# Kernel optimization log

Measured on AMD Instinct MI355X. Metric: run time of the kernel, lower is better.

Reference implementation:

```python
import jax, jax.numpy as jnp
import numpy as np

FRAME_NUMBER = 16
FRAME_SIZE = 128
SAMPLE_NUM = 16
NUM_EVENTS = 1048576


def setup_inputs() -> dict:
    key = jax.random.key(0)
    k1, k2, k3, k4 = jax.random.split(key, 4)
    event_values = jax.random.normal(k1, (SAMPLE_NUM, NUM_EVENTS), dtype=jnp.float32)
    # indices rows: (t, x, y). t sorted ascending so torch's `indices[0, -1] + 1`
    # sizing logic is valid; x, y in [0, FRAME_SIZE).
    t_idx = jnp.sort(jax.random.randint(k2, (NUM_EVENTS,), 0, NUM_EVENTS // FRAME_NUMBER, dtype=jnp.int64))
    x_idx = jax.random.randint(k3, (NUM_EVENTS,), 0, FRAME_SIZE, dtype=jnp.int64)
    y_idx = jax.random.randint(k4, (NUM_EVENTS,), 0, FRAME_SIZE, dtype=jnp.int64)
    idx0 = jnp.stack([t_idx, x_idx, y_idx], axis=0)  # [3, num_events]
    # Module only reads event_indices[0]; replicate across samples for shape fidelity.
    event_indices = jnp.broadcast_to(idx0[None], (SAMPLE_NUM, 3, NUM_EVENTS))
    return {"event_values": event_values, "event_indices": event_indices, "use_soft": 0}


def reference(event_values, event_indices, use_soft):
    # Hard split by number (use_soft=False path).
    # coalesce over (t,x,y) + sparse.sum over t == scatter-add over (x,y) per window.
    S, N = event_values.shape
    F, FS = FRAME_NUMBER, FRAME_SIZE
    W = N // F  # time_window (events per frame)

    x_idx = event_indices[0, 1]  # [N], shared across samples (module uses indices[0])
    y_idx = event_indices[0, 2]  # [N]
    frame_id = jnp.arange(N, dtype=x_idx.dtype) // W  # which frame each event falls in
    seg = (frame_id * FS + x_idx) * FS + y_idx  # flat (frame, x, y) bin id, [N]

    pos = jax.nn.relu(event_values)   # [S, N]
    neg = jax.nn.relu(-event_values)  # [S, N]

    num_segments = F * FS * FS
    # segment_sum over events -> [F*FS*FS, S], then reshape to [F, X, Y, S]
    pos_f = jax.ops.segment_sum(pos.T, seg, num_segments=num_segments).reshape(F, FS, FS, S)
    neg_f = jax.ops.segment_sum(neg.T, seg, num_segments=num_segments).reshape(F, FS, FS, S)

    frames = jnp.stack([neg_f, pos_f], axis=1)  # [F, 2, X, Y, S]
    # torch: permute(-1,0,1,3,2) -> [S,F,2,Y,X], then transpose(0,1) -> [F,S,2,Y,X]
    return jnp.transpose(frames, (0, 4, 1, 3, 2))
```

## Files before the change

kernel.cpp:

```cpp
#include <hip/hip_runtime.h>

#define SAMPLES 16
#define NEVENTS (1 << 20)
#define FRAMES  16
#define FSZ     128
#define WIN     (NEVENTS / FRAMES)
#define BINS    (FSZ * FSZ)
#define TPB     1024
#define EPT     16
#define STEPS   (WIN / (EPT * TPB))

typedef float v4f __attribute__((ext_vector_type(4)));
typedef int   v4i __attribute__((ext_vector_type(4)));


__device__ __forceinline__ void prep4(v4f v, v4i xv, v4i yv, int* off, float* av) {
    const unsigned ux = __float_as_uint(v.x), uy = __float_as_uint(v.y),
                   uz = __float_as_uint(v.z), uw = __float_as_uint(v.w);
    off[0] = (int)((((~ux) >> 31) << 14) | ((unsigned)yv.x << 7) | (unsigned)xv.x);
    off[1] = (int)((((~uy) >> 31) << 14) | ((unsigned)yv.y << 7) | (unsigned)xv.y);
    off[2] = (int)((((~uz) >> 31) << 14) | ((unsigned)yv.z << 7) | (unsigned)xv.z);
    off[3] = (int)((((~uw) >> 31) << 14) | ((unsigned)yv.w << 7) | (unsigned)xv.w);
    av[0] = __builtin_fabsf(v.x);
    av[1] = __builtin_fabsf(v.y);
    av[2] = __builtin_fabsf(v.z);
    av[3] = __builtin_fabsf(v.w);
}

#define LOADSTEP(B, step)                                                        \
    v##B##0 = __builtin_nontemporal_load(&ev4[(step) * 4 * TPB + 0 * TPB + tid]);\
    v##B##1 = __builtin_nontemporal_load(&ev4[(step) * 4 * TPB + 1 * TPB + tid]);\
    v##B##2 = __builtin_nontemporal_load(&ev4[(step) * 4 * TPB + 2 * TPB + tid]);\
    v##B##3 = __builtin_nontemporal_load(&ev4[(step) * 4 * TPB + 3 * TPB + tid]);\
    x##B##0 = x4[(step) * 4 * TPB + 0 * TPB + tid];                              \
    x##B##1 = x4[(step) * 4 * TPB + 1 * TPB + tid];                              \
    x##B##2 = x4[(step) * 4 * TPB + 2 * TPB + tid];                              \
    x##B##3 = x4[(step) * 4 * TPB + 3 * TPB + tid];                              \
    y##B##0 = y4[(step) * 4 * TPB + 0 * TPB + tid];                              \
    y##B##1 = y4[(step) * 4 * TPB + 1 * TPB + tid];                              \
    y##B##2 = y4[(step) * 4 * TPB + 2 * TPB + tid];                              \
    y##B##3 = y4[(step) * 4 * TPB + 3 * TPB + tid];

#define PREP(B)                                                                  \
    prep4(v##B##0, x##B##0, y##B##0, &off[0],  &av[0]);                          \
    prep4(v##B##1, x##B##1, y##B##1, &off[4],  &av[4]);                          \
    prep4(v##B##2, x##B##2, y##B##2, &off[8],  &av[8]);                          \
    prep4(v##B##3, x##B##3, y##B##3, &off[12], &av[12]);

#define BURST()                                                                  \
    _Pragma("unroll")                                                            \
    for (int k = 0; k < 16; ++k) atomicAdd(&lds[off[k]], av[k]);

__global__ __launch_bounds__(TPB) void frame_accum_kernel(
    const float* __restrict__ ev,
    const int*   __restrict__ idx,
    float*       __restrict__ out)
{
    extern __shared__ float lds[];
    const int tid = threadIdx.x;
    const int s = blockIdx.x & (SAMPLES - 1);
    const int f = blockIdx.x >> 4;

    v4f* lds4 = (v4f*)lds;
    const v4f zero4 = (v4f)(0.f);
#pragma unroll
    for (int i = 0; i < (2 * BINS / 4) / TPB; ++i)
        lds4[i * TPB + tid] = zero4;
    __syncthreads();

    const v4f* ev4 = (const v4f*)(ev  + (size_t)s * NEVENTS + (size_t)f * WIN);
    const v4i* x4  = (const v4i*)(idx + (size_t)NEVENTS      + (size_t)f * WIN);
    const v4i* y4  = (const v4i*)(idx + (size_t)2 * NEVENTS  + (size_t)f * WIN);

    v4f vA0, vA1, vA2, vA3, vB0, vB1, vB2, vB3;
    v4i xA0, xA1, xA2, xA3, xB0, xB1, xB2, xB3;
    v4i yA0, yA1, yA2, yA3, yB0, yB1, yB2, yB3;
    int   off[16];
    float av[16];

    LOADSTEP(A, 0)
#pragma unroll
    for (int st = 0; st < STEPS; st += 2) {
        LOADSTEP(B, st + 1)
        PREP(A)
        BURST()
        if (st + 2 < STEPS) { LOADSTEP(A, st + 2) }
        PREP(B)
        BURST()
    }
    __syncthreads();

    v4f* op4 = (v4f*)(out + ((size_t)(f * SAMPLES + s)) * 2 * BINS);
#pragma unroll
    for (int i = 0; i < (2 * BINS / 4) / TPB; ++i)
        __builtin_nontemporal_store(lds4[i * TPB + tid], &op4[i * TPB + tid]);
}

extern "C" void kernel_launch(void* const* d_in, const int* in_sizes, int n_in,
                              void* d_out, int out_size, void* d_ws, size_t ws_size,
                              hipStream_t stream) {
    const float* ev  = (const float*)d_in[0];
    const int*   idx = (const int*)d_in[1];
    float* out = (float*)d_out;

    (void)hipFuncSetAttribute((const void*)frame_accum_kernel,
                              hipFuncAttributeMaxDynamicSharedMemorySize,
                              2 * BINS * (int)sizeof(float));

    frame_accum_kernel<<<FRAMES * SAMPLES, TPB, 2 * BINS * sizeof(float), stream>>>(
        ev, idx, out);
}
```

Before: 343.9 us.

## Split atomic accumulation between LDS and global workspace atomics

Adds a hybrid kernel that sends odd chunks of events to global-memory atomics in a zeroed workspace and even chunks to LDS atomics, then sums both at the end. The goal is to spread atomic contention across two hardware paths instead of serializing everything on LDS atomics. The main loop is also simplified to single-vector chunks with unroll 4, replacing the manual double-buffered prefetch. The cost is an extra memset of the output-sized workspace, global atomic traffic through L2, and an extra workspace read. The hybrid path runs only when a large enough workspace is provided; otherwise an LDS-only fallback runs.

```diff
diff --git a/kernel.cpp b/kernel.cpp
--- a/kernel.cpp
+++ b/kernel.cpp
@@ -6,9 +6,12 @@
 #define FSZ     128
 #define WIN     (NEVENTS / FRAMES)
 #define BINS    (FSZ * FSZ)
+#define PLANES  2
+#define SLICE   (PLANES * BINS)
 #define TPB     1024
-#define EPT     16
-#define STEPS   (WIN / (EPT * TPB))
+#define CHUNKS  (WIN / (4 * TPB))
+#define OUTFLOATS ((size_t)FRAMES * SAMPLES * SLICE)
+#define OUTBYTES  (OUTFLOATS * sizeof(float))
 
 typedef float v4f __attribute__((ext_vector_type(4)));
 typedef int   v4i __attribute__((ext_vector_type(4)));
@@ -27,31 +30,62 @@
     av[3] = __builtin_fabsf(v.w);
 }
 
-#define LOADSTEP(B, step)                                                        \
-    v##B##0 = __builtin_nontemporal_load(&ev4[(step) * 4 * TPB + 0 * TPB + tid]);\
-    v##B##1 = __builtin_nontemporal_load(&ev4[(step) * 4 * TPB + 1 * TPB + tid]);\
-    v##B##2 = __builtin_nontemporal_load(&ev4[(step) * 4 * TPB + 2 * TPB + tid]);\
-    v##B##3 = __builtin_nontemporal_load(&ev4[(step) * 4 * TPB + 3 * TPB + tid]);\
-    x##B##0 = x4[(step) * 4 * TPB + 0 * TPB + tid];                              \
-    x##B##1 = x4[(step) * 4 * TPB + 1 * TPB + tid];                              \
-    x##B##2 = x4[(step) * 4 * TPB + 2 * TPB + tid];                              \
-    x##B##3 = x4[(step) * 4 * TPB + 3 * TPB + tid];                              \
-    y##B##0 = y4[(step) * 4 * TPB + 0 * TPB + tid];                              \
-    y##B##1 = y4[(step) * 4 * TPB + 1 * TPB + tid];                              \
-    y##B##2 = y4[(step) * 4 * TPB + 2 * TPB + tid];                              \
-    y##B##3 = y4[(step) * 4 * TPB + 3 * TPB + tid];
+__global__ __launch_bounds__(TPB) void frame_accum_hybrid(
+    const float* __restrict__ ev,
+    const int*   __restrict__ idx,
+    float*       __restrict__ ws,
+    float*       __restrict__ out)
+{
+    extern __shared__ float lds[];
+    const int tid = threadIdx.x;
+    const int s = blockIdx.x & (SAMPLES - 1);
+    const int f = blockIdx.x >> 4;
 
-#define PREP(B)                                                                  \
-    prep4(v##B##0, x##B##0, y##B##0, &off[0],  &av[0]);                          \
-    prep4(v##B##1, x##B##1, y##B##1, &off[4],  &av[4]);                          \
-    prep4(v##B##2, x##B##2, y##B##2, &off[8],  &av[8]);                          \
-    prep4(v##B##3, x##B##3, y##B##3, &off[12], &av[12]);
+    v4f* lds4 = (v4f*)lds;
+    const v4f zero4 = (v4f)(0.f);
+#pragma unroll
+    for (int i = 0; i < (SLICE / 4) / TPB; ++i)
+        lds4[i * TPB + tid] = zero4;
+    __syncthreads();
 
-#define BURST()                                                                  \
-    _Pragma("unroll")                                                            \
-    for (int k = 0; k < 16; ++k) atomicAdd(&lds[off[k]], av[k]);
+    const v4f* ev4 = (const v4f*)(ev  + (size_t)s * NEVENTS + (size_t)f * WIN);
+    const v4i* x4  = (const v4i*)(idx + (size_t)NEVENTS      + (size_t)f * WIN);
+    const v4i* y4  = (const v4i*)(idx + (size_t)2 * NEVENTS  + (size_t)f * WIN);
+    float* wsp = ws + (size_t)(f * SAMPLES + s) * SLICE;
 
-__global__ __launch_bounds__(TPB) void frame_accum_kernel(
+#pragma unroll 4
+    for (int c = 0; c < CHUNKS; ++c) {
+        const int base = c * TPB + tid;
+        const v4f v  = __builtin_nontemporal_load(&ev4[base]);
+        const v4i xv = x4[base];
+        const v4i yv = y4[base];
+        int off[4]; float av[4];
+        prep4(v, xv, yv, off, av);
+        if (c & 1) {
+#pragma unroll
+            for (int k = 0; k < 4; ++k)
+                (void)__hip_atomic_fetch_add(&wsp[off[k]], av[k],
+                                             __ATOMIC_RELAXED,
+                                             __HIP_MEMORY_SCOPE_WORKGROUP);
+        } else {
+#pragma unroll
+            for (int k = 0; k < 4; ++k)
+                atomicAdd(&lds[off[k]], av[k]);
+        }
+    }
+    __threadfence_block();
+    __syncthreads();
+
+    const v4f* ws4 = (const v4f*)wsp;
+    v4f* op4 = (v4f*)(out + (size_t)(f * SAMPLES + s) * SLICE);
+#pragma unroll
+    for (int i = 0; i < (SLICE / 4) / TPB; ++i) {
+        const v4f r = lds4[i * TPB + tid] + ws4[i * TPB + tid];
+        __builtin_nontemporal_store(r, &op4[i * TPB + tid]);
+    }
+}
+
+__global__ __launch_bounds__(TPB) void frame_accum_ldsonly(
     const float* __restrict__ ev,
     const int*   __restrict__ idx,
     float*       __restrict__ out)
@@ -64,7 +98,7 @@
     v4f* lds4 = (v4f*)lds;
     const v4f zero4 = (v4f)(0.f);
 #pragma unroll
-    for (int i = 0; i < (2 * BINS / 4) / TPB; ++i)
+    for (int i = 0; i < (SLICE / 4) / TPB; ++i)
         lds4[i * TPB + tid] = zero4;
     __syncthreads();
 
@@ -72,27 +106,23 @@
     const v4i* x4  = (const v4i*)(idx + (size_t)NEVENTS      + (size_t)f * WIN);
     const v4i* y4  = (const v4i*)(idx + (size_t)2 * NEVENTS  + (size_t)f * WIN);
 
-    v4f vA0, vA1, vA2, vA3, vB0, vB1, vB2, vB3;
-    v4i xA0, xA1, xA2, xA3, xB0, xB1, xB2, xB3;
-    v4i yA0, yA1, yA2, yA3, yB0, yB1, yB2, yB3;
-    int   off[16];
-    float av[16];
-
-    LOADSTEP(A, 0)
+#pragma unroll 4
+    for (int c = 0; c < CHUNKS; ++c) {
+        const int base = c * TPB + tid;
+        const v4f v  = __builtin_nontemporal_load(&ev4[base]);
+        const v4i xv = x4[base];
+        const v4i yv = y4[base];
+        int off[4]; float av[4];
+        prep4(v, xv, yv, off, av);
 #pragma unroll
-    for (int st = 0; st < STEPS; st += 2) {
-        LOADSTEP(B, st + 1)
-        PREP(A)
-        BURST()
-        if (st + 2 < STEPS) { LOADSTEP(A, st + 2) }
-        PREP(B)
-        BURST()
+        for (int k = 0; k < 4; ++k)
+            atomicAdd(&lds[off[k]], av[k]);
     }
     __syncthreads();
 
-    v4f* op4 = (v4f*)(out + ((size_t)(f * SAMPLES + s)) * 2 * BINS);
+    v4f* op4 = (v4f*)(out + (size_t)(f * SAMPLES + s) * SLICE);
 #pragma unroll
-    for (int i = 0; i < (2 * BINS / 4) / TPB; ++i)
+    for (int i = 0; i < (SLICE / 4) / TPB; ++i)
         __builtin_nontemporal_store(lds4[i * TPB + tid], &op4[i * TPB + tid]);
 }
 
@@ -103,10 +133,19 @@
     const int*   idx = (const int*)d_in[1];
     float* out = (float*)d_out;
 
-    (void)hipFuncSetAttribute((const void*)frame_accum_kernel,
-                              hipFuncAttributeMaxDynamicSharedMemorySize,
-                              2 * BINS * (int)sizeof(float));
-
-    frame_accum_kernel<<<FRAMES * SAMPLES, TPB, 2 * BINS * sizeof(float), stream>>>(
-        ev, idx, out);
+    if (d_ws != nullptr && ws_size >= OUTBYTES) {
+        float* ws = (float*)d_ws;
+        (void)hipMemsetAsync(ws, 0, OUTBYTES, stream);
+        (void)hipFuncSetAttribute((const void*)frame_accum_hybrid,
+                                  hipFuncAttributeMaxDynamicSharedMemorySize,
+                                  SLICE * (int)sizeof(float));
+        frame_accum_hybrid<<<FRAMES * SAMPLES, TPB, SLICE * sizeof(float), stream>>>(
+            ev, idx, ws, out);
+    } else {
+        (void)hipFuncSetAttribute((const void*)frame_accum_ldsonly,
+                                  hipFuncAttributeMaxDynamicSharedMemorySize,
+                                  SLICE * (int)sizeof(float));
+        frame_accum_ldsonly<<<FRAMES * SAMPLES, TPB, SLICE * sizeof(float), stream>>>(
+            ev, idx, out);
+    }
 }
```

Result: slower. 658.8 us (+91.6%).
